# Kernel tuning notes

Measured on AMD Instinct MI355X. Metric: run time of the kernel, lower is better.

## Reference

```python
import jax, jax.numpy as jnp
import numpy as np

BATCH = 2048
INPUT_DIM = 512
N = 8 ** 4  # reservoir_n ** reservoir_d = 4096
T = 16
NEG_SLOPE = 0.1
SPARSITY = 0.1  # fraction of nonzero entries in the pre-trained reservoir W


def setup_inputs() -> dict:
    key = jax.random.key(0)
    kx, kw, km = jax.random.split(key, 3)
    x = jax.random.normal(kx, (BATCH, INPUT_DIM), dtype=jnp.float32)
    # Sparse pre-trained reservoir weights; scale keeps spectral norm ~O(1)
    # so the T-step recurrence neither explodes nor vanishes.
    mask = (jax.random.uniform(km, (N, N)) < SPARSITY).astype(jnp.float32)
    W = jax.random.normal(kw, (N, N), dtype=jnp.float32) * mask / jnp.sqrt(SPARSITY * N)
    return {"x": x, "W": W}


def reference(x, W):
    # Pad input [B, input_dim] -> initial state S [B, N]
    S0 = jnp.pad(x, ((0, 0), (0, N - x.shape[1])))

    def step(S, _):
        S = jax.nn.leaky_relu(S @ W, negative_slope=NEG_SLOPE)
        return S, None

    S_final, _ = jax.lax.scan(step, S0, None, length=T)
    return S_final
```

## Files before the change

kernel.cpp:

```cpp
#include <hip/hip_runtime.h>


#define BATCH 2048
#define NDIM  4096
#define INDIM 512
#define BM 128
#define BN 128
#define BK 32

typedef _Float16 f16x8 __attribute__((ext_vector_type(8)));
typedef float    f32x4 __attribute__((ext_vector_type(4)));

__device__ __forceinline__ void async16(const void* gsrc, void* ldst) {
  const __attribute__((address_space(1))) unsigned int* g =
      (const __attribute__((address_space(1))) unsigned int*)gsrc;
  __attribute__((address_space(3))) unsigned int* l =
      (__attribute__((address_space(3))) unsigned int*)ldst;
  __builtin_amdgcn_global_load_lds(g, l, 16, 0, 0);
}

#define WAITV8() do { asm volatile("s_waitcnt vmcnt(8)" ::: "memory"); \
                      __builtin_amdgcn_sched_barrier(0); } while (0)
#define WAITV0() do { asm volatile("s_waitcnt vmcnt(0)" ::: "memory"); \
                      __builtin_amdgcn_sched_barrier(0); } while (0)
#define LGKM0()  do { asm volatile("s_waitcnt lgkmcnt(0)" ::: "memory"); \
                      __builtin_amdgcn_sched_barrier(0); } while (0)
#define SBAR()   __builtin_amdgcn_s_barrier()

__global__ void prep_x(const float* __restrict__ x,
                       _Float16* __restrict__ Sh, _Float16* __restrict__ Sl) {
  size_t i = (size_t)blockIdx.x * 256 + threadIdx.x;
  int b = (int)(i >> 12);
  int n = (int)(i & (NDIM - 1));
  float v = (n < INDIM) ? x[(size_t)b * INDIM + n] : 0.0f;
  _Float16 h = (_Float16)v;
  Sh[i] = h;
  Sl[i] = (_Float16)(v - (float)h);
}

__global__ void prep_w(const float* __restrict__ W,
                       _Float16* __restrict__ Wth, _Float16* __restrict__ Wtl) {
  __shared__ float tile[32][33];
  int k0 = blockIdx.y * 32, n0 = blockIdx.x * 32;
  int tx = threadIdx.x, ty = threadIdx.y;
  for (int r = 0; r < 4; r++) {
    int k = k0 + ty + r * 8;
    tile[ty + r * 8][tx] = W[(size_t)k * NDIM + n0 + tx];
  }
  __syncthreads();
  for (int r = 0; r < 4; r++) {
    int n = n0 + ty + r * 8;
    float v = tile[tx][ty + r * 8] * 256.0f;
    _Float16 h = (_Float16)v;
    Wth[(size_t)n * NDIM + k0 + tx] = h;
    Wtl[(size_t)n * NDIM + k0 + tx] = (_Float16)(v - (float)h);
  }
}

#define READF(b, A, L, Bv, M)                          \
  do {                                                 \
    _Pragma("unroll") for (int i = 0; i < 4; i++) {    \
      A[i]  = *(const f16x8*)&sAh[b][oA[i]];           \
      L[i]  = *(const f16x8*)&sAl[b][oA[i]];           \
      Bv[i] = *(const f16x8*)&sBh[b][oB[i]];           \
      M[i]  = *(const f16x8*)&sBl[b][oB[i]];           \
    }                                                  \
  } while (0)

#define MFMAS(A, L, Bv, M)                                                          \
  do {                                                                              \
    _Pragma("unroll") for (int j = 0; j < 4; j++)                                   \
    _Pragma("unroll") for (int i = 0; i < 4; i++) {                                 \
      acc[i][j] = __builtin_amdgcn_mfma_f32_16x16x32_f16(A[i], Bv[j], acc[i][j], 0, 0, 0); \
      acc[i][j] = __builtin_amdgcn_mfma_f32_16x16x32_f16(L[i], Bv[j], acc[i][j], 0, 0, 0); \
      acc[i][j] = __builtin_amdgcn_mfma_f32_16x16x32_f16(A[i], M[j], acc[i][j], 0, 0, 0); \
    }                                                                               \
  } while (0)

template <int MODE>
__global__ __launch_bounds__(256, 2) void step_kernel(
    const _Float16* __restrict__ Ah, const _Float16* __restrict__ Al,
    const _Float16* __restrict__ Bh, const _Float16* __restrict__ Bl,
    _Float16* __restrict__ Dh, _Float16* __restrict__ Dl,
    float* __restrict__ Dout, int k_len) {
  __shared__ _Float16 sAh[2][BM * BK];
  __shared__ _Float16 sAl[2][BM * BK];
  __shared__ _Float16 sBh[2][BN * BK];
  __shared__ _Float16 sBl[2][BN * BK];

  const int tid = threadIdx.x;
  const int lane = tid & 63;
  const int w = tid >> 6;
  const int wm = w >> 1, wn = w & 1;

  int id = blockIdx.x;
  int xcd = id & 7, local = id >> 3;
  int lr = local & 7, lc = local >> 3;
  const int bm = ((xcd & 1) * 8 + lr) * BM;
  const int bn = ((xcd >> 1) * 8 + lc) * BN;

  const int sr = lane >> 2, cl = lane & 3;
  const int fm = lane & 15, fq = lane >> 4;

  int oA[4], oB[4];
#pragma unroll
  for (int i = 0; i < 4; i++) {
    int rA = wm * 64 + i * 16 + fm;
    oA[i] = rA * BK + (fq ^ ((rA >> 1) & 3)) * 8;
    int rB = wn * 64 + i * 16 + fm;
    oB[i] = rB * BK + (fq ^ ((rB >> 1) & 3)) * 8;
  }

  int r0 = w * 32 + sr, r1 = r0 + 16;
  int cg0 = cl ^ ((r0 >> 1) & 3);
  int cg1 = cl ^ ((r1 >> 1) & 3);
  const size_t gA0 = (size_t)(bm + r0) * NDIM + cg0 * 8;
  const size_t gA1 = (size_t)(bm + r1) * NDIM + cg1 * 8;
  const size_t gB0 = (size_t)(bn + r0) * NDIM + cg0 * 8;
  const size_t gB1 = (size_t)(bn + r1) * NDIM + cg1 * 8;
  const int lo0 = r0 * BK + cl * 8;
  const int lo1 = r1 * BK + cl * 8;

  auto stage = [&](int kt, int b) {
    async16(Ah + gA0 + kt, &sAh[b][lo0]);
    async16(Ah + gA1 + kt, &sAh[b][lo1]);
    async16(Al + gA0 + kt, &sAl[b][lo0]);
    async16(Al + gA1 + kt, &sAl[b][lo1]);
    async16(Bh + gB0 + kt, &sBh[b][lo0]);
    async16(Bh + gB1 + kt, &sBh[b][lo1]);
    async16(Bl + gB0 + kt, &sBl[b][lo0]);
    async16(Bl + gB1 + kt, &sBl[b][lo1]);
  };

  f32x4 acc[4][4];
#pragma unroll
  for (int i = 0; i < 4; i++)
#pragma unroll
    for (int j = 0; j < 4; j++) acc[i][j] = (f32x4){0.f, 0.f, 0.f, 0.f};

  f16x8 a0[4], l0[4], b0[4], m0[4];
  f16x8 a1[4], l1[4], b1[4], m1[4];

  const int nk = k_len / BK;

  stage(0 * BK, 0);
  stage(1 * BK, 1);
  WAITV8(); SBAR();
  READF(0, a0, l0, b0, m0);
  LGKM0(); SBAR();
  stage(2 * BK, 0);

  int it = 1;
  for (; it + 1 < nk; it += 2) {
    WAITV8(); SBAR();
    READF(1, a1, l1, b1, m1);
    MFMAS(a0, l0, b0, m0);
    LGKM0(); SBAR();
    if (it + 2 < nk) stage((it + 2) * BK, 1);

    WAITV8(); SBAR();
    READF(0, a0, l0, b0, m0);
    MFMAS(a1, l1, b1, m1);
    LGKM0(); SBAR();
    if (it + 3 < nk) stage((it + 3) * BK, 0);
  }
  WAITV0(); SBAR();
  READF(1, a1, l1, b1, m1);
  MFMAS(a0, l0, b0, m0);
  LGKM0();
  MFMAS(a1, l1, b1, m1);

  const float inv = 1.0f / 256.0f;
#pragma unroll
  for (int i = 0; i < 4; i++) {
#pragma unroll
    for (int j = 0; j < 4; j++) {
#pragma unroll
      for (int e = 0; e < 4; e++) {
        int r = bm + wm * 64 + i * 16 + fq * 4 + e;
        int c = bn + wn * 64 + j * 16 + fm;
        float g = acc[i][j][e] * inv;
        float s = (g > 0.0f) ? g : 0.1f * g;
        if (MODE == 0) {
          _Float16 h = (_Float16)s;
          Dh[(size_t)r * NDIM + c] = h;
          Dl[(size_t)r * NDIM + c] = (_Float16)(s - (float)h);
        } else {
          Dout[(size_t)r * NDIM + c] = s;
        }
      }
    }
  }
}

extern "C" void kernel_launch(void* const* d_in, const int* in_sizes, int n_in,
                              void* d_out, int out_size, void* d_ws, size_t ws_size,
                              hipStream_t stream) {
  const float* x = (const float*)d_in[0];
  const float* W = (const float*)d_in[1];
  float* out = (float*)d_out;
  char* ws = (char*)d_ws;

  const size_t WT_BYTES = (size_t)NDIM * NDIM * 2;
  const size_t S_BYTES = (size_t)BATCH * NDIM * 2;
  _Float16* Wth = (_Float16*)ws;
  _Float16* Wtl = (_Float16*)(ws + WT_BYTES);
  _Float16* SAh = (_Float16*)(ws + 2 * WT_BYTES);
  _Float16* SAl = (_Float16*)(ws + 2 * WT_BYTES + S_BYTES);
  _Float16* SBh = (_Float16*)(ws + 2 * WT_BYTES + 2 * S_BYTES);
  _Float16* SBl = (_Float16*)(ws + 2 * WT_BYTES + 3 * S_BYTES);

  prep_x<<<(BATCH * NDIM) / 256, 256, 0, stream>>>(x, SAh, SAl);
  prep_w<<<dim3(NDIM / 32, NDIM / 32), dim3(32, 8), 0, stream>>>(W, Wth, Wtl);

  dim3 grid((NDIM / BN) * (BATCH / BM));
  for (int t = 1; t <= 16; t++) {
    const _Float16* ah = (t & 1) ? SAh : SBh;
    const _Float16* al = (t & 1) ? SAl : SBl;
    _Float16* dh = (t & 1) ? SBh : SAh;
    _Float16* dl = (t & 1) ? SBl : SAl;
    int klen = (t == 1) ? INDIM : NDIM;
    if (t < 16)
      step_kernel<0><<<grid, 256, 0, stream>>>(ah, al, Wth, Wtl, dh, dl, nullptr, klen);
    else
      step_kernel<1><<<grid, 256, 0, stream>>>(ah, al, Wth, Wtl, nullptr, nullptr, out, klen);
  }
}
```

Measured before the change: 2.407 ms.

## Prepack W in MFMA fragment layout and load B operands directly to registers

prep_w now writes the transposed, 256-scaled hi/lo halves of W in a blocked layout that matches the 16x16x32 MFMA B-fragment order. The step kernel then loads B fragments straight from global memory into registers one k-step ahead, instead of staging them through LDS. This drops half the LDS traffic and footprint, and the LDS reads for B. The vmcnt waits are retuned to match the new load counts, and the MFMA issue order is regrouped by product term. In exchange, the two waves that share a column tile each fetch the same B data from L2, and global-load latency now sits closer to the MFMAs.

```diff
diff --git a/kernel.cpp b/kernel.cpp
--- a/kernel.cpp
+++ b/kernel.cpp
@@ -8,6 +8,7 @@
 #define BN 128
 #define BK 32
 
+typedef _Float16 f16x4 __attribute__((ext_vector_type(4)));
 typedef _Float16 f16x8 __attribute__((ext_vector_type(8)));
 typedef float    f32x4 __attribute__((ext_vector_type(4)));
 
@@ -19,13 +20,13 @@
   __builtin_amdgcn_global_load_lds(g, l, 16, 0, 0);
 }
 
-#define WAITV8() do { asm volatile("s_waitcnt vmcnt(8)" ::: "memory"); \
-                      __builtin_amdgcn_sched_barrier(0); } while (0)
-#define WAITV0() do { asm volatile("s_waitcnt vmcnt(0)" ::: "memory"); \
-                      __builtin_amdgcn_sched_barrier(0); } while (0)
-#define LGKM0()  do { asm volatile("s_waitcnt lgkmcnt(0)" ::: "memory"); \
-                      __builtin_amdgcn_sched_barrier(0); } while (0)
-#define SBAR()   __builtin_amdgcn_s_barrier()
+#define WAITV12() do { asm volatile("s_waitcnt vmcnt(12)" ::: "memory"); \
+                       __builtin_amdgcn_sched_barrier(0); } while (0)
+#define WAITV8()  do { asm volatile("s_waitcnt vmcnt(8)" ::: "memory");  \
+                       __builtin_amdgcn_sched_barrier(0); } while (0)
+#define LGKM0()   do { asm volatile("s_waitcnt lgkmcnt(0)" ::: "memory"); \
+                       __builtin_amdgcn_sched_barrier(0); } while (0)
+#define SBAR()    __builtin_amdgcn_s_barrier()
 
 __global__ void prep_x(const float* __restrict__ x,
                        _Float16* __restrict__ Sh, _Float16* __restrict__ Sl) {
@@ -41,40 +42,62 @@
 __global__ void prep_w(const float* __restrict__ W,
                        _Float16* __restrict__ Wth, _Float16* __restrict__ Wtl) {
   __shared__ float tile[32][33];
-  int k0 = blockIdx.y * 32, n0 = blockIdx.x * 32;
+  int nb2 = blockIdx.x, ktb = blockIdx.y;
+  int k0 = ktb * 32, n0 = nb2 * 32;
   int tx = threadIdx.x, ty = threadIdx.y;
   for (int r = 0; r < 4; r++) {
-    int k = k0 + ty + r * 8;
-    tile[ty + r * 8][tx] = W[(size_t)k * NDIM + n0 + tx];
+    int kl = ty + r * 8;
+    tile[kl][tx] = W[(size_t)(k0 + kl) * NDIM + n0 + tx];
   }
   __syncthreads();
-  for (int r = 0; r < 4; r++) {
-    int n = n0 + ty + r * 8;
-    float v = tile[tx][ty + r * 8] * 256.0f;
+  int tid = ty * 32 + tx;
+  int r2 = tid >> 7;
+  int t128 = tid & 127;
+  int L = t128 >> 1;
+  int e0 = (t128 & 1) * 4;
+  int fq = L >> 4, fm = L & 15;
+  int nl = r2 * 16 + fm;
+  f16x4 hi4, lo4;
+#pragma unroll
+  for (int q = 0; q < 4; q++) {
+    float v = tile[fq * 8 + e0 + q][nl] * 256.0f;
     _Float16 h = (_Float16)v;
-    Wth[(size_t)n * NDIM + k0 + tx] = h;
-    Wtl[(size_t)n * NDIM + k0 + tx] = (_Float16)(v - (float)h);
-  }
-}
-
-#define READF(b, A, L, Bv, M)                          \
+    hi4[q] = h;
+    lo4[q] = (_Float16)(v - (float)h);
+  }
+  size_t base = (((size_t)(nb2 * 2 + r2) * 128 + ktb) << 9) + L * 8 + e0;
+  *(f16x4*)&Wth[base] = hi4;
+  *(f16x4*)&Wtl[base] = lo4;
+}
+
+#define READFA(b, A, L)                                \
   do {                                                 \
     _Pragma("unroll") for (int i = 0; i < 4; i++) {    \
-      A[i]  = *(const f16x8*)&sAh[b][oA[i]];           \
-      L[i]  = *(const f16x8*)&sAl[b][oA[i]];           \
-      Bv[i] = *(const f16x8*)&sBh[b][oB[i]];           \
-      M[i]  = *(const f16x8*)&sBl[b][oB[i]];           \
+      A[i] = *(const f16x8*)&sAh[b][oA[i]];            \
+      L[i] = *(const f16x8*)&sAl[b][oA[i]];            \
+    }                                                  \
+  } while (0)
+
+#define LOADB(Bv, M, kt)                               \
+  do {                                                 \
+    _Pragma("unroll") for (int j = 0; j < 4; j++) {    \
+      size_t g = gB[j] + ((size_t)(kt) << 9);          \
+      Bv[j] = *(const f16x8*)&Bh[g];                   \
+      M[j]  = *(const f16x8*)&Bl[g];                   \
     }                                                  \
   } while (0)
 
 #define MFMAS(A, L, Bv, M)                                                          \
   do {                                                                              \
     _Pragma("unroll") for (int j = 0; j < 4; j++)                                   \
-    _Pragma("unroll") for (int i = 0; i < 4; i++) {                                 \
+    _Pragma("unroll") for (int i = 0; i < 4; i++)                                   \
       acc[i][j] = __builtin_amdgcn_mfma_f32_16x16x32_f16(A[i], Bv[j], acc[i][j], 0, 0, 0); \
+    _Pragma("unroll") for (int j = 0; j < 4; j++)                                   \
+    _Pragma("unroll") for (int i = 0; i < 4; i++)                                   \
       acc[i][j] = __builtin_amdgcn_mfma_f32_16x16x32_f16(L[i], Bv[j], acc[i][j], 0, 0, 0); \
+    _Pragma("unroll") for (int j = 0; j < 4; j++)                                   \
+    _Pragma("unroll") for (int i = 0; i < 4; i++)                                   \
       acc[i][j] = __builtin_amdgcn_mfma_f32_16x16x32_f16(A[i], M[j], acc[i][j], 0, 0, 0); \
-    }                                                                               \
   } while (0)
 
 template <int MODE>
@@ -85,8 +108,6 @@
     float* __restrict__ Dout, int k_len) {
   __shared__ _Float16 sAh[2][BM * BK];
   __shared__ _Float16 sAl[2][BM * BK];
-  __shared__ _Float16 sBh[2][BN * BK];
-  __shared__ _Float16 sBl[2][BN * BK];
 
   const int tid = threadIdx.x;
   const int lane = tid & 63;
@@ -102,13 +123,18 @@
   const int sr = lane >> 2, cl = lane & 3;
   const int fm = lane & 15, fq = lane >> 4;
 
-  int oA[4], oB[4];
+  int oA[4];
 #pragma unroll
   for (int i = 0; i < 4; i++) {
     int rA = wm * 64 + i * 16 + fm;
     oA[i] = rA * BK + (fq ^ ((rA >> 1) & 3)) * 8;
-    int rB = wn * 64 + i * 16 + fm;
-    oB[i] = rB * BK + (fq ^ ((rB >> 1) & 3)) * 8;
+  }
+
+  size_t gB[4];
+#pragma unroll
+  for (int j = 0; j < 4; j++) {
+    int nbB = (bn >> 4) + wn * 4 + j;
+    gB[j] = ((size_t)nbB << 16) + lane * 8;
   }
 
   int r0 = w * 32 + sr, r1 = r0 + 16;
@@ -116,8 +142,6 @@
   int cg1 = cl ^ ((r1 >> 1) & 3);
   const size_t gA0 = (size_t)(bm + r0) * NDIM + cg0 * 8;
   const size_t gA1 = (size_t)(bm + r1) * NDIM + cg1 * 8;
-  const size_t gB0 = (size_t)(bn + r0) * NDIM + cg0 * 8;
-  const size_t gB1 = (size_t)(bn + r1) * NDIM + cg1 * 8;
   const int lo0 = r0 * BK + cl * 8;
   const int lo1 = r1 * BK + cl * 8;
 
@@ -126,10 +150,6 @@
     async16(Ah + gA1 + kt, &sAh[b][lo1]);
     async16(Al + gA0 + kt, &sAl[b][lo0]);
     async16(Al + gA1 + kt, &sAl[b][lo1]);
-    async16(Bh + gB0 + kt, &sBh[b][lo0]);
-    async16(Bh + gB1 + kt, &sBh[b][lo1]);
-    async16(Bl + gB0 + kt, &sBl[b][lo0]);
-    async16(Bl + gB1 + kt, &sBl[b][lo1]);
   };
 
   f32x4 acc[4][4];
@@ -145,27 +165,31 @@
 
   stage(0 * BK, 0);
   stage(1 * BK, 1);
-  WAITV8(); SBAR();
-  READF(0, a0, l0, b0, m0);
+  LOADB(b0, m0, 0);
+  WAITV12(); SBAR();
+  READFA(0, a0, l0);
   LGKM0(); SBAR();
   stage(2 * BK, 0);
 
   int it = 1;
   for (; it + 1 < nk; it += 2) {
-    WAITV8(); SBAR();
-    READF(1, a1, l1, b1, m1);
+    WAITV12(); SBAR();
+    LOADB(b1, m1, it);
+    READFA(1, a1, l1);
     MFMAS(a0, l0, b0, m0);
     LGKM0(); SBAR();
     if (it + 2 < nk) stage((it + 2) * BK, 1);
 
-    WAITV8(); SBAR();
-    READF(0, a0, l0, b0, m0);
+    WAITV12(); SBAR();
+    LOADB(b0, m0, it + 1);
+    READFA(0, a0, l0);
     MFMAS(a1, l1, b1, m1);
     LGKM0(); SBAR();
     if (it + 3 < nk) stage((it + 3) * BK, 0);
   }
-  WAITV0(); SBAR();
-  READF(1, a1, l1, b1, m1);
+  WAITV8(); SBAR();
+  LOADB(b1, m1, nk - 1);
+  READFA(1, a1, l1);
   MFMAS(a0, l0, b0, m0);
   LGKM0();
   MFMAS(a1, l1, b1, m1);
```

Result: slower. 2.486 ms (+3.3%).

## Use 512-thread blocks with 8 waves and single-buffered register fragments

Applied to the files above, without the earlier changes.

Doubles the waves per 128x128 block to 8 (2x4 layout), so each wave computes a 64x32 sub-tile with half the accumulators and B fragments. The register double-buffered fragment pipeline is replaced by a simple loop that reads fragments, issues the next async stage, then runs the MFMAs, with a vmcnt(4) wait to match the halved per-thread load count. The aim is to lower register pressure and raise occupancy so more waves hide latency. In exchange, each wave reuses fragments less and loses the overlap between LDS reads and MFMAs within a wave.

```diff
diff --git a/kernel.cpp b/kernel.cpp
--- a/kernel.cpp
+++ b/kernel.cpp
@@ -19,7 +19,7 @@
   __builtin_amdgcn_global_load_lds(g, l, 16, 0, 0);
 }
 
-#define WAITV8() do { asm volatile("s_waitcnt vmcnt(8)" ::: "memory"); \
+#define WAITV4() do { asm volatile("s_waitcnt vmcnt(4)" ::: "memory"); \
                       __builtin_amdgcn_sched_barrier(0); } while (0)
 #define WAITV0() do { asm volatile("s_waitcnt vmcnt(0)" ::: "memory"); \
                       __builtin_amdgcn_sched_barrier(0); } while (0)
@@ -57,28 +57,33 @@
   }
 }
 
-#define READF(b, A, L, Bv, M)                          \
+#define READF(b)                                       \
   do {                                                 \
     _Pragma("unroll") for (int i = 0; i < 4; i++) {    \
-      A[i]  = *(const f16x8*)&sAh[b][oA[i]];           \
-      L[i]  = *(const f16x8*)&sAl[b][oA[i]];           \
-      Bv[i] = *(const f16x8*)&sBh[b][oB[i]];           \
-      M[i]  = *(const f16x8*)&sBl[b][oB[i]];           \
+      af[i] = *(const f16x8*)&sAh[b][oA[i]];           \
+      lf[i] = *(const f16x8*)&sAl[b][oA[i]];           \
+    }                                                  \
+    _Pragma("unroll") for (int j = 0; j < 2; j++) {    \
+      bf[j] = *(const f16x8*)&sBh[b][oB[j]];           \
+      mf[j] = *(const f16x8*)&sBl[b][oB[j]];           \
     }                                                  \
   } while (0)
 
-#define MFMAS(A, L, Bv, M)                                                          \
+#define MFMAS()                                                                     \
   do {                                                                              \
-    _Pragma("unroll") for (int j = 0; j < 4; j++)                                   \
-    _Pragma("unroll") for (int i = 0; i < 4; i++) {                                 \
-      acc[i][j] = __builtin_amdgcn_mfma_f32_16x16x32_f16(A[i], Bv[j], acc[i][j], 0, 0, 0); \
-      acc[i][j] = __builtin_amdgcn_mfma_f32_16x16x32_f16(L[i], Bv[j], acc[i][j], 0, 0, 0); \
-      acc[i][j] = __builtin_amdgcn_mfma_f32_16x16x32_f16(A[i], M[j], acc[i][j], 0, 0, 0); \
-    }                                                                               \
+    _Pragma("unroll") for (int j = 0; j < 2; j++)                                   \
+    _Pragma("unroll") for (int i = 0; i < 4; i++)                                   \
+      acc[i][j] = __builtin_amdgcn_mfma_f32_16x16x32_f16(af[i], bf[j], acc[i][j], 0, 0, 0); \
+    _Pragma("unroll") for (int j = 0; j < 2; j++)                                   \
+    _Pragma("unroll") for (int i = 0; i < 4; i++)                                   \
+      acc[i][j] = __builtin_amdgcn_mfma_f32_16x16x32_f16(lf[i], bf[j], acc[i][j], 0, 0, 0); \
+    _Pragma("unroll") for (int j = 0; j < 2; j++)                                   \
+    _Pragma("unroll") for (int i = 0; i < 4; i++)                                   \
+      acc[i][j] = __builtin_amdgcn_mfma_f32_16x16x32_f16(af[i], mf[j], acc[i][j], 0, 0, 0); \
   } while (0)
 
 template <int MODE>
-__global__ __launch_bounds__(256, 2) void step_kernel(
+__global__ __launch_bounds__(512, 4) void step_kernel(
     const _Float16* __restrict__ Ah, const _Float16* __restrict__ Al,
     const _Float16* __restrict__ Bh, const _Float16* __restrict__ Bl,
     _Float16* __restrict__ Dh, _Float16* __restrict__ Dl,
@@ -91,7 +96,7 @@
   const int tid = threadIdx.x;
   const int lane = tid & 63;
   const int w = tid >> 6;
-  const int wm = w >> 1, wn = w & 1;
+  const int wm = w >> 2, wn = w & 3;
 
   int id = blockIdx.x;
   int xcd = id & 7, local = id >> 3;
@@ -102,83 +107,62 @@
   const int sr = lane >> 2, cl = lane & 3;
   const int fm = lane & 15, fq = lane >> 4;
 
-  int oA[4], oB[4];
+  int oA[4], oB[2];
 #pragma unroll
   for (int i = 0; i < 4; i++) {
     int rA = wm * 64 + i * 16 + fm;
     oA[i] = rA * BK + (fq ^ ((rA >> 1) & 3)) * 8;
-    int rB = wn * 64 + i * 16 + fm;
-    oB[i] = rB * BK + (fq ^ ((rB >> 1) & 3)) * 8;
-  }
-
-  int r0 = w * 32 + sr, r1 = r0 + 16;
+  }
+#pragma unroll
+  for (int j = 0; j < 2; j++) {
+    int rB = wn * 32 + j * 16 + fm;
+    oB[j] = rB * BK + (fq ^ ((rB >> 1) & 3)) * 8;
+  }
+
+  int r0 = w * 16 + sr;
   int cg0 = cl ^ ((r0 >> 1) & 3);
-  int cg1 = cl ^ ((r1 >> 1) & 3);
   const size_t gA0 = (size_t)(bm + r0) * NDIM + cg0 * 8;
-  const size_t gA1 = (size_t)(bm + r1) * NDIM + cg1 * 8;
   const size_t gB0 = (size_t)(bn + r0) * NDIM + cg0 * 8;
-  const size_t gB1 = (size_t)(bn + r1) * NDIM + cg1 * 8;
   const int lo0 = r0 * BK + cl * 8;
-  const int lo1 = r1 * BK + cl * 8;
 
   auto stage = [&](int kt, int b) {
     async16(Ah + gA0 + kt, &sAh[b][lo0]);
-    async16(Ah + gA1 + kt, &sAh[b][lo1]);
     async16(Al + gA0 + kt, &sAl[b][lo0]);
-    async16(Al + gA1 + kt, &sAl[b][lo1]);
     async16(Bh + gB0 + kt, &sBh[b][lo0]);
-    async16(Bh + gB1 + kt, &sBh[b][lo1]);
     async16(Bl + gB0 + kt, &sBl[b][lo0]);
-    async16(Bl + gB1 + kt, &sBl[b][lo1]);
   };
 
-  f32x4 acc[4][4];
+  f32x4 acc[4][2];
 #pragma unroll
   for (int i = 0; i < 4; i++)
 #pragma unroll
-    for (int j = 0; j < 4; j++) acc[i][j] = (f32x4){0.f, 0.f, 0.f, 0.f};
-
-  f16x8 a0[4], l0[4], b0[4], m0[4];
-  f16x8 a1[4], l1[4], b1[4], m1[4];
+    for (int j = 0; j < 2; j++) acc[i][j] = (f32x4){0.f, 0.f, 0.f, 0.f};
+
+  f16x8 af[4], lf[4], bf[2], mf[2];
 
   const int nk = k_len / BK;
 
   stage(0 * BK, 0);
   stage(1 * BK, 1);
-  WAITV8(); SBAR();
-  READF(0, a0, l0, b0, m0);
-  LGKM0(); SBAR();
-  stage(2 * BK, 0);
-
-  int it = 1;
-  for (; it + 1 < nk; it += 2) {
-    WAITV8(); SBAR();
-    READF(1, a1, l1, b1, m1);
-    MFMAS(a0, l0, b0, m0);
+  for (int it = 0; it < nk; ++it) {
+    const int p = it & 1;
+    if (it + 1 < nk) { WAITV4(); } else { WAITV0(); }
+    SBAR();
+    READF(p);
     LGKM0(); SBAR();
-    if (it + 2 < nk) stage((it + 2) * BK, 1);
-
-    WAITV8(); SBAR();
-    READF(0, a0, l0, b0, m0);
-    MFMAS(a1, l1, b1, m1);
-    LGKM0(); SBAR();
-    if (it + 3 < nk) stage((it + 3) * BK, 0);
-  }
-  WAITV0(); SBAR();
-  READF(1, a1, l1, b1, m1);
-  MFMAS(a0, l0, b0, m0);
-  LGKM0();
-  MFMAS(a1, l1, b1, m1);
+    if (it + 2 < nk) stage((it + 2) * BK, p);
+    MFMAS();
+  }
 
   const float inv = 1.0f / 256.0f;
 #pragma unroll
   for (int i = 0; i < 4; i++) {
 #pragma unroll
-    for (int j = 0; j < 4; j++) {
+    for (int j = 0; j < 2; j++) {
 #pragma unroll
       for (int e = 0; e < 4; e++) {
         int r = bm + wm * 64 + i * 16 + fq * 4 + e;
-        int c = bn + wn * 64 + j * 16 + fm;
+        int c = bn + wn * 32 + j * 16 + fm;
         float g = acc[i][j][e] * inv;
         float s = (g > 0.0f) ? g : 0.1f * g;
         if (MODE == 0) {
@@ -221,8 +205,8 @@
     _Float16* dl = (t & 1) ? SBl : SAl;
     int klen = (t == 1) ? INDIM : NDIM;
     if (t < 16)
-      step_kernel<0><<<grid, 256, 0, stream>>>(ah, al, Wth, Wtl, dh, dl, nullptr, klen);
+      step_kernel<0><<<grid, 512, 0, stream>>>(ah, al, Wth, Wtl, dh, dl, nullptr, klen);
     else
-      step_kernel<1><<<grid, 256, 0, stream>>>(ah, al, Wth, Wtl, nullptr, nullptr, out, klen);
-  }
-}
+      step_kernel<1><<<grid, 512, 0, stream>>>(ah, al, Wth, Wtl, nullptr, nullptr, out, klen);
+  }
+}
```

Result: slower. 2.491 ms (+3.5%).
